# Optimization experiments

Measured on AMD Instinct MI355X. Metric: run time of the kernel, lower is better.

## Reference

```python
import jax, jax.numpy as jnp
import numpy as np
import math

B, S, E, H = 2, 2048, 1024, 16


def setup_inputs() -> dict:
    key = jax.random.key(0)
    ks = jax.random.split(key, 9)
    std = 0.02
    return {
        "x": jax.random.normal(ks[0], (B, S, E), dtype=jnp.float32),
        "Wq": jax.random.normal(ks[1], (E, E), dtype=jnp.float32) * std,
        "bq": jnp.zeros((E,), dtype=jnp.float32),
        "Wk": jax.random.normal(ks[2], (E, E), dtype=jnp.float32) * std,
        "bk": jnp.zeros((E,), dtype=jnp.float32),
        "Wv": jax.random.normal(ks[3], (E, E), dtype=jnp.float32) * std,
        "bv": jnp.zeros((E,), dtype=jnp.float32),
        "Wfc": jax.random.normal(ks[4], (E, E), dtype=jnp.float32) * std,
        "bfc": jnp.zeros((E,), dtype=jnp.float32),
        "n_head": H,
    }


def reference(x, Wq, bq, Wk, bk, Wv, bv, Wfc, bfc, n_head):
    Bn, Sn, En = x.shape
    Hd = En // n_head  # head_dim
    # torch Linear: y = x @ W.T + b
    def proj(W, b):
        return (x @ W.T + b).reshape(Bn, Sn, n_head, Hd).transpose(0, 2, 1, 3)  # [B,H,S,D]
    q = proj(Wq, bq)
    k = proj(Wk, bk)
    v = proj(Wv, bv)
    scores = jnp.einsum('bhqd,bhkd->bhqk', q, k) / math.sqrt(Hd)  # [B,H,S,S]
    # ALiBi: slopes_h = 2^{-(h+1)}; alibi[h,i,j] = -slope_h * (i - j)
    slopes = 2.0 ** (-jnp.arange(1, n_head + 1, dtype=jnp.float32))  # [H]
    pos = jnp.arange(Sn, dtype=jnp.float32)
    rel = pos[:, None] - pos[None, :]  # [S,S], memory_pos - context_pos
    alibi = -slopes[:, None, None] * rel  # [H,S,S]
    scores = scores + alibi[None]
    weights = jax.nn.softmax(scores, axis=-1)  # [B,H,S,S]
    out = jnp.einsum('bhqk,bhkd->bqhd', weights, v).reshape(Bn, Sn, En)
    out = out @ Wfc.T + bfc
    return (out, weights)
```

## Files before the change

### kernel.cpp

```cpp
#include <hip/hip_runtime.h>
#include <hip/hip_bf16.h>
#include <cstdint>
#include <cstddef>

#define BB 2
#define SS 2048
#define EE 1024
#define HH 16
#define MM (BB*SS)

typedef __bf16 bf16;
typedef __bf16 bf16x8 __attribute__((ext_vector_type(8)));
typedef float f32x4 __attribute__((ext_vector_type(4)));

#define GLD16(gsrc, ldst) \
  __builtin_amdgcn_global_load_lds((const __attribute__((address_space(1))) void*)(gsrc), \
                                   (__attribute__((address_space(3))) void*)(ldst), 16, 0, 0)

__global__ __launch_bounds__(256) void cvt_f32_bf16(const float* __restrict__ src,
                                                    bf16* __restrict__ dst, int n) {
    int i = (blockIdx.x * 256 + threadIdx.x) * 8;
    if (i >= n) return;
    float4 a = *(const float4*)(src + i);
    float4 b = *(const float4*)(src + i + 4);
    bf16 o[8] = {(bf16)a.x,(bf16)a.y,(bf16)a.z,(bf16)a.w,
                 (bf16)b.x,(bf16)b.y,(bf16)b.z,(bf16)b.w};
    *(uint4*)(dst + i) = *(uint4*)o;
}

__global__ __launch_bounds__(256) void cvt4(const float* __restrict__ a, const float* __restrict__ b,
                                            const float* __restrict__ c, const float* __restrict__ d,
                                            bf16* __restrict__ oa, bf16* __restrict__ ob,
                                            bf16* __restrict__ oc, bf16* __restrict__ od) {
    int sel = blockIdx.y;
    const float* s = sel == 0 ? a : sel == 1 ? b : sel == 2 ? c : d;
    bf16* o       = sel == 0 ? oa : sel == 1 ? ob : sel == 2 ? oc : od;
    int i = (blockIdx.x * 256 + threadIdx.x) * 8;
    float4 x = *(const float4*)(s + i);
    float4 y = *(const float4*)(s + i + 4);
    bf16 t[8] = {(bf16)x.x,(bf16)x.y,(bf16)x.z,(bf16)x.w,
                 (bf16)y.x,(bf16)y.y,(bf16)y.z,(bf16)y.w};
    *(uint4*)(o + i) = *(uint4*)t;
}

template<int MODE>
__global__ __launch_bounds__(256) void gemm128(const bf16* __restrict__ A,
                                               const bf16* __restrict__ W0,
                                               const bf16* __restrict__ W1,
                                               const bf16* __restrict__ W2,
                                               const float* __restrict__ b0,
                                               const float* __restrict__ b1,
                                               const float* __restrict__ b2,
                                               void* __restrict__ o0,
                                               void* __restrict__ o1,
                                               void* __restrict__ o2) {
    __shared__ bf16 Al[128*64];
    __shared__ bf16 Bl[128*64];
    const int t = threadIdx.x;
    const int wsel = blockIdx.x >> 3;
    const int n0 = (blockIdx.x & 7) * 128;
    const int m0 = blockIdx.y * 128;
    const bf16* W  = wsel == 0 ? W0 : wsel == 1 ? W1 : W2;
    const float* bias = wsel == 0 ? b0 : wsel == 1 ? b1 : b2;
    void* outp = wsel == 0 ? o0 : wsel == 1 ? o1 : o2;

    const int w = t >> 6, lane = t & 63, lg = lane >> 4, li = lane & 15;
    const int wr = w >> 1, wc = w & 1;
    f32x4 acc[4][4] = {};

    for (int k0 = 0; k0 < 1024; k0 += 64) {
        __syncthreads();
        #pragma unroll
        for (int i = 0; i < 4; ++i) {
            int f = i * 256 + t;
            int row = f >> 3, c = (f & 7) * 8;
            GLD16(A + (size_t)(m0 + row) * 1024 + k0 + c, Al + f * 8);
            GLD16(W + (size_t)(n0 + row) * 1024 + k0 + c, Bl + f * 8);
        }
        __syncthreads();
        #pragma unroll
        for (int ks = 0; ks < 2; ++ks) {
            bf16x8 af[4], bf_[4];
            #pragma unroll
            for (int m = 0; m < 4; ++m)
                af[m] = *(const bf16x8*)&Al[(wr*64 + m*16 + li)*64 + ks*32 + lg*8];
            #pragma unroll
            for (int n = 0; n < 4; ++n)
                bf_[n] = *(const bf16x8*)&Bl[(wc*64 + n*16 + li)*64 + ks*32 + lg*8];
            #pragma unroll
            for (int m = 0; m < 4; ++m)
                #pragma unroll
                for (int n = 0; n < 4; ++n)
                    acc[m][n] = __builtin_amdgcn_mfma_f32_16x16x32_bf16(af[m], bf_[n], acc[m][n], 0,0,0);
        }
    }
    #pragma unroll
    for (int m = 0; m < 4; ++m)
      #pragma unroll
      for (int n = 0; n < 4; ++n)
        #pragma unroll
        for (int r = 0; r < 4; ++r) {
            int row = m0 + wr*64 + m*16 + lg*4 + r;
            int col = n0 + wc*64 + n*16 + li;
            float v = acc[m][n][r] + bias[col];
            if (MODE == 0) {
                int b = row >> 11, s = row & (SS-1);
                int h = col >> 6, d = col & 63;
                ((bf16*)outp)[(((size_t)(b*HH + h)*SS + s) << 6) + d] = (bf16)v;
            } else {
                ((float*)outp)[(size_t)row*1024 + col] = v;
            }
        }
}

__global__ __launch_bounds__(256) void transpose_v(const bf16* __restrict__ V,
                                                   bf16* __restrict__ Vt) {
    __shared__ bf16 L[64][72];
    const int bh = blockIdx.y, s0 = blockIdx.x * 64, t = threadIdx.x;
    for (int id = t; id < 512; id += 256) {
        int row = id >> 3, c = id & 7;
        *(uint4*)&L[row][c*8] = *(const uint4*)&V[((size_t)bh*SS + s0 + row)*64 + c*8];
    }
    __syncthreads();
    for (int id = t; id < 512; id += 256) {
        int d = id >> 3, c = id & 7;
        bf16 tmp[8];
        #pragma unroll
        for (int jj = 0; jj < 8; ++jj) tmp[jj] = L[c*8 + jj][d];
        *(uint4*)&Vt[((size_t)bh*64 + d)*SS + s0 + c*8] = *(uint4*)tmp;
    }
}

__global__ __launch_bounds__(256) void attn1_kernel(const bf16* __restrict__ Q,
                                                    const bf16* __restrict__ Kk,
                                                    const bf16* __restrict__ Vt,
                                                    float* __restrict__ Lbuf,
                                                    bf16* __restrict__ aout) {
    __shared__ bf16 ring[4][64*64];
    __shared__ float Lred[2][64];

    const int lin = blockIdx.x + (int)(gridDim.x * blockIdx.y);
    const int nl  = (lin & 7) * 128 + (lin >> 3);
    const int qt = nl & 31, bh = nl >> 5;

    const int b = bh >> 4, h = bh & 15;
    const int q0 = qt * 64;
    const int t = threadIdx.x, w = t >> 6, lane = t & 63, lg = lane >> 4, li = lane & 15;
    const int jh = w & 1, qh = w >> 1;
    const float slope = exp2f(-(float)(h + 1));
    const size_t kvbase = (size_t)bh * SS * 64;
    const size_t vtbase = (size_t)bh * 64 * SS;
    const float L2E = 1.4426950408889634f;
    const float K1 = 0.125f * L2E;
    const float C  = slope * L2E;
    const float C64 = C * 64.f;

    bf16x8 aq[2][2];
    #pragma unroll
    for (int cbq = 0; cbq < 2; ++cbq) {
        const bf16* qptr = Q + kvbase + (size_t)(q0 + qh*32 + cbq*16 + li) * 64;
        aq[cbq][0] = *(const bf16x8*)(qptr + lg*8);
        aq[cbq][1] = *(const bf16x8*)(qptr + 32 + lg*8);
    }
    const int swz = (li & 7) << 4;

    #define STAGE_K(J0, DST) do {                                              \
        _Pragma("unroll")                                                      \
        for (int i_ = 0; i_ < 2; ++i_) {                                       \
            int f_ = i_*256 + t; int row_ = f_ >> 3, c_ = f_ & 7;              \
            GLD16(Kk + kvbase + (size_t)((J0) + row_)*64 + (c_ ^ (row_ & 7))*8,\
                  (DST) + f_*8);                                               \
        } } while (0)
    #define STAGE_V(J0, DST) do {                                              \
        _Pragma("unroll")                                                      \
        for (int i_ = 0; i_ < 2; ++i_) {                                       \
            int f_ = i_*256 + t; int row_ = f_ >> 3, c_ = f_ & 7;              \
            GLD16(Vt + vtbase + (size_t)row_*SS + (J0) + (c_ ^ (row_ & 7))*8,  \
                  (DST) + f_*8);                                               \
        } } while (0)

    float cj[2][4];
    #pragma unroll
    for (int jt = 0; jt < 2; ++jt)
        #pragma unroll
        for (int r = 0; r < 4; ++r)
            cj[jt][r] = C * (float)(jh*32 + jt*16 + lg*4 + r - (SS-1));
    float lp[2] = {0.f, 0.f};
    f32x4 acc[2][4] = {};

    STAGE_K(0, &ring[0][0]);
    STAGE_V(0, &ring[2][0]);
    __syncthreads();
    for (int kt = 0; kt < 32; ++kt) {
        const int cur = kt & 1;
        const int j0 = kt * 64;
        if (kt + 1 < 32) {
            STAGE_K(j0 + 64, &ring[cur ^ 1][0]);
            STAGE_V(j0 + 64, &ring[2 + (cur ^ 1)][0]);
        }
        const char* Ksb = (const char*)&ring[cur][0];
        const char* Vsb = (const char*)&ring[2 + cur][0];
        bf16x8 ak[2][2];
        #pragma unroll
        for (int jt = 0; jt < 2; ++jt) {
            int row = jh*32 + jt*16 + li;
            ak[jt][0] = *(const bf16x8*)(Ksb + row*128 + ((     lg*16) ^ swz));
            ak[jt][1] = *(const bf16x8*)(Ksb + row*128 + ((64 + lg*16) ^ swz));
        }
        f32x4 sc[2][2] = {};
        __builtin_amdgcn_s_setprio(1);
        #pragma unroll
        for (int jt = 0; jt < 2; ++jt)
            #pragma unroll
            for (int cbq = 0; cbq < 2; ++cbq) {
                sc[jt][cbq] = __builtin_amdgcn_mfma_f32_16x16x32_bf16(ak[jt][0], aq[cbq][0], sc[jt][cbq], 0,0,0);
                sc[jt][cbq] = __builtin_amdgcn_mfma_f32_16x16x32_bf16(ak[jt][1], aq[cbq][1], sc[jt][cbq], 0,0,0);
            }
        __builtin_amdgcn_s_setprio(0);
        f32x4 wv[2][2];
        #pragma unroll
        for (int jt = 0; jt < 2; ++jt) {
            #pragma unroll
            for (int cbq = 0; cbq < 2; ++cbq) {
                f32x4 v;
                #pragma unroll
                for (int r = 0; r < 4; ++r) {
                    v[r] = __builtin_amdgcn_exp2f(fmaf(sc[jt][cbq][r], K1, cj[jt][r]));
                    lp[cbq] += v[r];
                }
                wv[jt][cbq] = v;
            }
            #pragma unroll
            for (int r = 0; r < 4; ++r) cj[jt][r] += C64;
        }
        bf16x8 pa[2];
        #pragma unroll
        for (int cbq = 0; cbq < 2; ++cbq) {
            bf16x8 p;
            p[0] = (bf16)wv[0][cbq][0]; p[1] = (bf16)wv[0][cbq][1];
            p[2] = (bf16)wv[0][cbq][2]; p[3] = (bf16)wv[0][cbq][3];
            p[4] = (bf16)wv[1][cbq][0]; p[5] = (bf16)wv[1][cbq][1];
            p[6] = (bf16)wv[1][cbq][2]; p[7] = (bf16)wv[1][cbq][3];
            pa[cbq] = p;
        }
        bf16x8 vb[4];
        #pragma unroll
        for (int d0 = 0; d0 < 4; ++d0) {
            int row = d0*16 + li;
            uint2 u0 = *(const uint2*)(Vsb + row*128 + ((jh*64      + lg*8) ^ swz));
            uint2 u1 = *(const uint2*)(Vsb + row*128 + ((jh*64 + 32 + lg*8) ^ swz));
            uint4 uu = {u0.x, u0.y, u1.x, u1.y};
            vb[d0] = __builtin_bit_cast(bf16x8, uu);
        }
        __builtin_amdgcn_s_setprio(1);
        #pragma unroll
        for (int cbq = 0; cbq < 2; ++cbq)
            #pragma unroll
            for (int d0 = 0; d0 < 4; ++d0)
                acc[cbq][d0] = __builtin_amdgcn_mfma_f32_16x16x32_bf16(pa[cbq], vb[d0], acc[cbq][d0], 0,0,0);
        __builtin_amdgcn_s_setprio(0);
        __syncthreads();
    }
    #pragma unroll
    for (int cbq = 0; cbq < 2; ++cbq) {
        lp[cbq] += __shfl_xor(lp[cbq], 16);
        lp[cbq] += __shfl_xor(lp[cbq], 32);
    }
    if (lg == 0) {
        Lred[jh][qh*32 + li]      = lp[0];
        Lred[jh][qh*32 + 16 + li] = lp[1];
    }
    __syncthreads();
    if (t < 64) {
        float lv = Lred[0][t] + Lred[1][t];
        Lbuf[(size_t)bh*SS + q0 + t] = __builtin_amdgcn_logf(lv);
    }
    float rinv2[2][4];
    #pragma unroll
    for (int cbq = 0; cbq < 2; ++cbq)
        #pragma unroll
        for (int r = 0; r < 4; ++r) {
            int qi = qh*32 + cbq*16 + lg*4 + r;
            rinv2[cbq][r] = 1.f / (Lred[0][qi] + Lred[1][qi]);
        }
    __syncthreads();

    bf16* Obuf = &ring[0][0];
    #pragma unroll
    for (int cbq = 0; cbq < 2; ++cbq)
        #pragma unroll
        for (int d0 = 0; d0 < 4; ++d0)
            #pragma unroll
            for (int r = 0; r < 4; ++r)
                Obuf[jh*4096 + (qh*32 + cbq*16 + lg*4 + r)*64 + d0*16 + li] =
                    (bf16)(acc[cbq][d0][r] * rinv2[cbq][r]);
    __syncthreads();
    {
        int q = t >> 2, dc = (t & 3) << 4;
        const bf16* o0 = Obuf +        q*64 + dc;
        const bf16* o1 = Obuf + 4096 + q*64 + dc;
        bf16x8 a0 = *(const bf16x8*)(o0),     a1 = *(const bf16x8*)(o0 + 8);
        bf16x8 b0 = *(const bf16x8*)(o1),     b1 = *(const bf16x8*)(o1 + 8);
        bf16 ov[16];
        #pragma unroll
        for (int e = 0; e < 8; ++e) {
            ov[e]     = (bf16)((float)a0[e] + (float)b0[e]);
            ov[8 + e] = (bf16)((float)a1[e] + (float)b1[e]);
        }
        bf16* dst = aout + ((size_t)(b*SS + q0 + q))*EE + h*64 + dc;
        *(uint4*)(dst)     = *(uint4*)(ov);
        *(uint4*)(dst + 8) = *(uint4*)(ov + 8);
    }
    #undef STAGE_K
    #undef STAGE_V
}

__global__ __launch_bounds__(256) void weights_kernel(const bf16* __restrict__ Q,
                                                      const bf16* __restrict__ Kk,
                                                      const float* __restrict__ Lbuf,
                                                      float* __restrict__ wout) {
    const int lin = blockIdx.x + (int)(gridDim.x * blockIdx.y);
    const int nl  = (lin & 7) * 256 + (lin >> 3);
    const int bh = nl >> 6, rr = nl & 63;
    const int qt = rr >> 1, jc = rr & 1;

    const int h = bh & 15;
    const int q0 = qt * 64;
    const int jbase = jc * 1024;
    const int t = threadIdx.x, w = t >> 6, lane = t & 63, lg = lane >> 4, li = lane & 15;
    const int jh = w & 1, qh = w >> 1;
    const float slope = exp2f(-(float)(h + 1));
    const size_t kvbase = (size_t)bh * SS * 64;
    const float L2E = 1.4426950408889634f;
    const float K1 = 0.125f * L2E;
    const float C  = slope * L2E;
    const float C64 = C * 64.f;

    bf16x8 aq[2][2];
    float lgl[2];
    #pragma unroll
    for (int cbq = 0; cbq < 2; ++cbq) {
        const int qi = q0 + qh*32 + cbq*16 + li;
        const bf16* qptr = Q + kvbase + (size_t)qi * 64;
        aq[cbq][0] = *(const bf16x8*)(qptr + lg*8);
        aq[cbq][1] = *(const bf16x8*)(qptr + 32 + lg*8);
        lgl[cbq] = Lbuf[(size_t)bh*SS + qi];
    }
    float ecr[2][2][4];
    #pragma unroll
    for (int jt = 0; jt < 2; ++jt)
        #pragma unroll
        for (int cbq = 0; cbq < 2; ++cbq)
            #pragma unroll
            for (int r = 0; r < 4; ++r)
                ecr[jt][cbq][r] = C * (float)(jbase + jh*32 + jt*16 + lg*4 + r - (SS-1)) - lgl[cbq];

    float* wrow0 = wout + ((size_t)bh*SS + q0 + qh*32 +      li) * SS;
    float* wrow1 = wout + ((size_t)bh*SS + q0 + qh*32 + 16 + li) * SS;

    #pragma unroll 2
    for (int kt = 0; kt < 16; ++kt) {
        const int j0 = jbase + kt * 64;
        bf16x8 ak[2][2];
        #pragma unroll
        for (int jt = 0; jt < 2; ++jt) {
            const bf16* kr = Kk + kvbase + (size_t)(j0 + jh*32 + jt*16 + li) * 64;
            ak[jt][0] = *(const bf16x8*)(kr + lg*8);
            ak[jt][1] = *(const bf16x8*)(kr + 32 + lg*8);
        }
        f32x4 sc[2][2] = {};
        #pragma unroll
        for (int jt = 0; jt < 2; ++jt)
            #pragma unroll
            for (int cbq = 0; cbq < 2; ++cbq) {
                sc[jt][cbq] = __builtin_amdgcn_mfma_f32_16x16x32_bf16(ak[jt][0], aq[cbq][0], sc[jt][cbq], 0,0,0);
                sc[jt][cbq] = __builtin_amdgcn_mfma_f32_16x16x32_bf16(ak[jt][1], aq[cbq][1], sc[jt][cbq], 0,0,0);
            }
        #pragma unroll
        for (int jt = 0; jt < 2; ++jt)
            #pragma unroll
            for (int cbq = 0; cbq < 2; ++cbq) {
                f32x4 v;
                v[0] = __builtin_amdgcn_exp2f(fmaf(sc[jt][cbq][0], K1, ecr[jt][cbq][0]));
                v[1] = __builtin_amdgcn_exp2f(fmaf(sc[jt][cbq][1], K1, ecr[jt][cbq][1]));
                v[2] = __builtin_amdgcn_exp2f(fmaf(sc[jt][cbq][2], K1, ecr[jt][cbq][2]));
                v[3] = __builtin_amdgcn_exp2f(fmaf(sc[jt][cbq][3], K1, ecr[jt][cbq][3]));
                float* wr = (cbq == 0 ? wrow0 : wrow1);
                __builtin_nontemporal_store(v, (f32x4*)&wr[j0 + jh*32 + jt*16 + lg*4]);
                ecr[jt][cbq][0] += C64; ecr[jt][cbq][1] += C64;
                ecr[jt][cbq][2] += C64; ecr[jt][cbq][3] += C64;
            }
    }
}

extern "C" void kernel_launch(void* const* d_in, const int* in_sizes, int n_in,
                              void* d_out, int out_size, void* d_ws, size_t ws_size,
                              hipStream_t stream) {
    const float* x   = (const float*)d_in[0];
    const float* Wq  = (const float*)d_in[1];
    const float* bq  = (const float*)d_in[2];
    const float* Wk  = (const float*)d_in[3];
    const float* bk  = (const float*)d_in[4];
    const float* Wv  = (const float*)d_in[5];
    const float* bv  = (const float*)d_in[6];
    const float* Wfc = (const float*)d_in[7];
    const float* bfc = (const float*)d_in[8];

    char* ws = (char*)d_ws;
    const size_t MB = 1024u*1024u;
    bf16* xb   = (bf16*)(ws + 0);
    bf16* wqb  = (bf16*)(ws + 8*MB);
    bf16* wkb  = (bf16*)(ws + 10*MB);
    bf16* wvb  = (bf16*)(ws + 12*MB);
    bf16* wfb  = (bf16*)(ws + 14*MB);
    bf16* Qb   = (bf16*)(ws + 16*MB);
    bf16* Kb   = (bf16*)(ws + 24*MB);
    bf16* Vb   = (bf16*)(ws + 32*MB);
    bf16* Vtb  = (bf16*)(ws + 40*MB);
    bf16* Ab   = (bf16*)(ws + 48*MB);
    float* Lb  = (float*)(ws + 0);

    float* outp = (float*)d_out;
    float* wout = outp + (size_t)BB*SS*EE;

    cvt_f32_bf16<<<dim3(4194304/8/256), 256, 0, stream>>>(x, xb, 4194304);
    cvt4<<<dim3(512, 4), 256, 0, stream>>>(Wq, Wk, Wv, Wfc, wqb, wkb, wvb, wfb);

    gemm128<0><<<dim3(24, 32), 256, 0, stream>>>(xb, wqb, wkb, wvb, bq, bk, bv, Qb, Kb, Vb);

    transpose_v<<<dim3(SS/64, BB*HH), 256, 0, stream>>>(Vb, Vtb);

    attn1_kernel<<<dim3(32, 32), 256, 0, stream>>>(Qb, Kb, Vtb, Lb, Ab);

    weights_kernel<<<dim3(64, 32), 256, 0, stream>>>(Qb, Kb, Lb, wout);

    gemm128<1><<<dim3(8, 32), 256, 0, stream>>>(Ab, wfb, wfb, wfb, bfc, bfc, bfc, d_out, d_out, d_out);
}
```

Measured before the change: 341.4 us.

## Fuse PV into the weights-writing pass and split the key range across blocks

The attention stage is reorganised into four kernels. A light pass computes partial softmax denominators over two key halves, and a tiny kernel combines them into log-sums. The main kernel then writes the normalized attention weights and accumulates P·V in the same loop, each block handling half of the keys. A final kernel adds the two bf16 partial outputs. The goal is to overlap the PV MFMA work with the store-bound weights write and to double the number of blocks. In exchange it adds two small launches, extra partial-output traffic, and bf16 rounding of the partial sums.

New measurement: 319.8 us. 1.07x faster.

```diff
diff --git a/kernel.cpp b/kernel.cpp
--- a/kernel.cpp
+++ b/kernel.cpp
@@ -131,20 +131,127 @@
     }
 }
 
-__global__ __launch_bounds__(256) void attn1_kernel(const bf16* __restrict__ Q,
-                                                    const bf16* __restrict__ Kk,
-                                                    const bf16* __restrict__ Vt,
-                                                    float* __restrict__ Lbuf,
-                                                    bf16* __restrict__ aout) {
+__global__ __launch_bounds__(256) void lsum_kernel(const bf16* __restrict__ Q,
+                                                   const bf16* __restrict__ Kk,
+                                                   float* __restrict__ Lpart) {
+    __shared__ bf16 ring[2][64*64];
+    __shared__ float Lred[2][64];
+
+    const int lin = blockIdx.x + (int)(gridDim.x * blockIdx.y);
+    const int nl  = (lin & 7) * 256 + (lin >> 3);
+    const int bh = nl >> 6, rr = nl & 63;
+    const int qt = rr >> 1, jh2 = rr & 1;
+
+    const int h = bh & 15;
+    const int q0 = qt * 64;
+    const int jbase = jh2 * 1024;
+    const int t = threadIdx.x, w = t >> 6, lane = t & 63, lg = lane >> 4, li = lane & 15;
+    const int jh = w & 1, qh = w >> 1;
+    const float slope = exp2f(-(float)(h + 1));
+    const size_t kvbase = (size_t)bh * SS * 64;
+    const float L2E = 1.4426950408889634f;
+    const float K1 = 0.125f * L2E;
+    const float C  = slope * L2E;
+    const float C64 = C * 64.f;
+
+    bf16x8 aq[2][2];
+    #pragma unroll
+    for (int cbq = 0; cbq < 2; ++cbq) {
+        const bf16* qptr = Q + kvbase + (size_t)(q0 + qh*32 + cbq*16 + li) * 64;
+        aq[cbq][0] = *(const bf16x8*)(qptr + lg*8);
+        aq[cbq][1] = *(const bf16x8*)(qptr + 32 + lg*8);
+    }
+    const int swz = (li & 7) << 4;
+
+    #define STAGE_K(J0, DST) do {                                              \
+        _Pragma("unroll")                                                      \
+        for (int i_ = 0; i_ < 2; ++i_) {                                       \
+            int f_ = i_*256 + t; int row_ = f_ >> 3, c_ = f_ & 7;              \
+            GLD16(Kk + kvbase + (size_t)((J0) + row_)*64 + (c_ ^ (row_ & 7))*8,\
+                  (DST) + f_*8);                                               \
+        } } while (0)
+
+    float cj[2][4];
+    #pragma unroll
+    for (int jt = 0; jt < 2; ++jt)
+        #pragma unroll
+        for (int r = 0; r < 4; ++r)
+            cj[jt][r] = C * (float)(jbase + jh*32 + jt*16 + lg*4 + r - (SS-1));
+    float lp[2] = {0.f, 0.f};
+
+    STAGE_K(jbase, &ring[0][0]);
+    __syncthreads();
+    for (int kt = 0; kt < 16; ++kt) {
+        const int cur = kt & 1;
+        if (kt + 1 < 16) STAGE_K(jbase + (kt+1)*64, &ring[cur ^ 1][0]);
+        const char* Ksb = (const char*)&ring[cur][0];
+        bf16x8 ak[2][2];
+        #pragma unroll
+        for (int jt = 0; jt < 2; ++jt) {
+            int row = jh*32 + jt*16 + li;
+            ak[jt][0] = *(const bf16x8*)(Ksb + row*128 + ((     lg*16) ^ swz));
+            ak[jt][1] = *(const bf16x8*)(Ksb + row*128 + ((64 + lg*16) ^ swz));
+        }
+        f32x4 sc[2][2] = {};
+        __builtin_amdgcn_s_setprio(1);
+        #pragma unroll
+        for (int jt = 0; jt < 2; ++jt)
+            #pragma unroll
+            for (int cbq = 0; cbq < 2; ++cbq) {
+                sc[jt][cbq] = __builtin_amdgcn_mfma_f32_16x16x32_bf16(ak[jt][0], aq[cbq][0], sc[jt][cbq], 0,0,0);
+                sc[jt][cbq] = __builtin_amdgcn_mfma_f32_16x16x32_bf16(ak[jt][1], aq[cbq][1], sc[jt][cbq], 0,0,0);
+            }
+        __builtin_amdgcn_s_setprio(0);
+        #pragma unroll
+        for (int jt = 0; jt < 2; ++jt) {
+            #pragma unroll
+            for (int cbq = 0; cbq < 2; ++cbq)
+                #pragma unroll
+                for (int r = 0; r < 4; ++r)
+                    lp[cbq] += __builtin_amdgcn_exp2f(fmaf(sc[jt][cbq][r], K1, cj[jt][r]));
+            #pragma unroll
+            for (int r = 0; r < 4; ++r) cj[jt][r] += C64;
+        }
+        __syncthreads();
+    }
+    #pragma unroll
+    for (int cbq = 0; cbq < 2; ++cbq) {
+        lp[cbq] += __shfl_xor(lp[cbq], 16);
+        lp[cbq] += __shfl_xor(lp[cbq], 32);
+    }
+    if (lg == 0) {
+        Lred[jh][qh*32 + li]      = lp[0];
+        Lred[jh][qh*32 + 16 + li] = lp[1];
+    }
+    __syncthreads();
+    if (t < 64)
+        Lpart[((size_t)(jh2*32 + bh))*SS + q0 + t] = Lred[0][t] + Lred[1][t];
+    #undef STAGE_K
+}
+
+__global__ __launch_bounds__(1024) void lfix_kernel(const float* __restrict__ Lpart,
+                                                    float* __restrict__ Lbuf) {
+    int i = blockIdx.x * 1024 + threadIdx.x;
+    Lbuf[i] = __builtin_amdgcn_logf(Lpart[i] + Lpart[65536 + i]);
+}
+
+__global__ __launch_bounds__(256) void wpv_kernel(const bf16* __restrict__ Q,
+                                                  const bf16* __restrict__ Kk,
+                                                  const bf16* __restrict__ Vt,
+                                                  const float* __restrict__ Lbuf,
+                                                  float* __restrict__ wout,
+                                                  bf16* __restrict__ opart0,
+                                                  bf16* __restrict__ opart1) {
     __shared__ bf16 ring[4][64*64];
-    __shared__ float Lred[2][64];
 
     const int lin = blockIdx.x + (int)(gridDim.x * blockIdx.y);
-    const int nl  = (lin & 7) * 128 + (lin >> 3);
-    const int qt = nl & 31, bh = nl >> 5;
+    const int nl  = (lin & 7) * 256 + (lin >> 3);
+    const int bh = nl >> 6, rr = nl & 63;
+    const int qt = rr >> 1, jh2 = rr & 1;
 
     const int b = bh >> 4, h = bh & 15;
     const int q0 = qt * 64;
+    const int jbase = jh2 * 1024;
     const int t = threadIdx.x, w = t >> 6, lane = t & 63, lg = lane >> 4, li = lane & 15;
     const int jh = w & 1, qh = w >> 1;
     const float slope = exp2f(-(float)(h + 1));
@@ -154,13 +261,17 @@
     const float K1 = 0.125f * L2E;
     const float C  = slope * L2E;
     const float C64 = C * 64.f;
+    bf16* opart = jh2 == 0 ? opart0 : opart1;
 
     bf16x8 aq[2][2];
+    float lgl[2];
     #pragma unroll
     for (int cbq = 0; cbq < 2; ++cbq) {
-        const bf16* qptr = Q + kvbase + (size_t)(q0 + qh*32 + cbq*16 + li) * 64;
+        const int qi = q0 + qh*32 + cbq*16 + li;
+        const bf16* qptr = Q + kvbase + (size_t)qi * 64;
         aq[cbq][0] = *(const bf16x8*)(qptr + lg*8);
         aq[cbq][1] = *(const bf16x8*)(qptr + 32 + lg*8);
+        lgl[cbq] = Lbuf[(size_t)bh*SS + qi];
     }
     const int swz = (li & 7) << 4;
 
@@ -179,22 +290,26 @@
                   (DST) + f_*8);                                               \
         } } while (0)
 
-    float cj[2][4];
+    float ecr[2][2][4];
     #pragma unroll
     for (int jt = 0; jt < 2; ++jt)
         #pragma unroll
-        for (int r = 0; r < 4; ++r)
-            cj[jt][r] = C * (float)(jh*32 + jt*16 + lg*4 + r - (SS-1));
-    float lp[2] = {0.f, 0.f};
+        for (int cbq = 0; cbq < 2; ++cbq)
+            #pragma unroll
+            for (int r = 0; r < 4; ++r)
+                ecr[jt][cbq][r] = C * (float)(jbase + jh*32 + jt*16 + lg*4 + r - (SS-1)) - lgl[cbq];
+
     f32x4 acc[2][4] = {};
-
-    STAGE_K(0, &ring[0][0]);
-    STAGE_V(0, &ring[2][0]);
+    float* wrow0 = wout + ((size_t)bh*SS + q0 + qh*32 +      li) * SS;
+    float* wrow1 = wout + ((size_t)bh*SS + q0 + qh*32 + 16 + li) * SS;
+
+    STAGE_K(jbase, &ring[0][0]);
+    STAGE_V(jbase, &ring[2][0]);
     __syncthreads();
-    for (int kt = 0; kt < 32; ++kt) {
+    for (int kt = 0; kt < 16; ++kt) {
         const int cur = kt & 1;
-        const int j0 = kt * 64;
-        if (kt + 1 < 32) {
+        const int j0 = jbase + kt * 64;
+        if (kt + 1 < 16) {
             STAGE_K(j0 + 64, &ring[cur ^ 1][0]);
             STAGE_V(j0 + 64, &ring[2 + (cur ^ 1)][0]);
         }
@@ -219,20 +334,20 @@
         __builtin_amdgcn_s_setprio(0);
         f32x4 wv[2][2];
         #pragma unroll
-        for (int jt = 0; jt < 2; ++jt) {
+        for (int jt = 0; jt < 2; ++jt)
             #pragma unroll
             for (int cbq = 0; cbq < 2; ++cbq) {
                 f32x4 v;
-                #pragma unroll
-                for (int r = 0; r < 4; ++r) {
-                    v[r] = __builtin_amdgcn_exp2f(fmaf(sc[jt][cbq][r], K1, cj[jt][r]));
-                    lp[cbq] += v[r];
-                }
+                v[0] = __builtin_amdgcn_exp2f(fmaf(sc[jt][cbq][0], K1, ecr[jt][cbq][0]));
+                v[1] = __builtin_amdgcn_exp2f(fmaf(sc[jt][cbq][1], K1, ecr[jt][cbq][1]));
+                v[2] = __builtin_amdgcn_exp2f(fmaf(sc[jt][cbq][2], K1, ecr[jt][cbq][2]));
+                v[3] = __builtin_amdgcn_exp2f(fmaf(sc[jt][cbq][3], K1, ecr[jt][cbq][3]));
                 wv[jt][cbq] = v;
+                float* wr = (cbq == 0 ? wrow0 : wrow1);
+                __builtin_nontemporal_store(v, (f32x4*)&wr[j0 + jh*32 + jt*16 + lg*4]);
+                ecr[jt][cbq][0] += C64; ecr[jt][cbq][1] += C64;
+                ecr[jt][cbq][2] += C64; ecr[jt][cbq][3] += C64;
             }
-            #pragma unroll
-            for (int r = 0; r < 4; ++r) cj[jt][r] += C64;
-        }
         bf16x8 pa[2];
         #pragma unroll
         for (int cbq = 0; cbq < 2; ++cbq) {
@@ -261,29 +376,6 @@
         __builtin_amdgcn_s_setprio(0);
         __syncthreads();
     }
-    #pragma unroll
-    for (int cbq = 0; cbq < 2; ++cbq) {
-        lp[cbq] += __shfl_xor(lp[cbq], 16);
-        lp[cbq] += __shfl_xor(lp[cbq], 32);
-    }
-    if (lg == 0) {
-        Lred[jh][qh*32 + li]      = lp[0];
-        Lred[jh][qh*32 + 16 + li] = lp[1];
-    }
-    __syncthreads();
-    if (t < 64) {
-        float lv = Lred[0][t] + Lred[1][t];
-        Lbuf[(size_t)bh*SS + q0 + t] = __builtin_amdgcn_logf(lv);
-    }
-    float rinv2[2][4];
-    #pragma unroll
-    for (int cbq = 0; cbq < 2; ++cbq)
-        #pragma unroll
-        for (int r = 0; r < 4; ++r) {
-            int qi = qh*32 + cbq*16 + lg*4 + r;
-            rinv2[cbq][r] = 1.f / (Lred[0][qi] + Lred[1][qi]);
-        }
-    __syncthreads();
 
     bf16* Obuf = &ring[0][0];
     #pragma unroll
@@ -293,7 +385,7 @@
             #pragma unroll
             for (int r = 0; r < 4; ++r)
                 Obuf[jh*4096 + (qh*32 + cbq*16 + lg*4 + r)*64 + d0*16 + li] =
-                    (bf16)(acc[cbq][d0][r] * rinv2[cbq][r]);
+                    (bf16)acc[cbq][d0][r];
     __syncthreads();
     {
         int q = t >> 2, dc = (t & 3) << 4;
@@ -307,7 +399,7 @@
             ov[e]     = (bf16)((float)a0[e] + (float)b0[e]);
             ov[8 + e] = (bf16)((float)a1[e] + (float)b1[e]);
         }
-        bf16* dst = aout + ((size_t)(b*SS + q0 + q))*EE + h*64 + dc;
+        bf16* dst = opart + ((size_t)(b*SS + q0 + q))*EE + h*64 + dc;
         *(uint4*)(dst)     = *(uint4*)(ov);
         *(uint4*)(dst + 8) = *(uint4*)(ov + 8);
     }
@@ -315,82 +407,16 @@
     #undef STAGE_V
 }
 
-__global__ __launch_bounds__(256) void weights_kernel(const bf16* __restrict__ Q,
-                                                      const bf16* __restrict__ Kk,
-                                                      const float* __restrict__ Lbuf,
-                                                      float* __restrict__ wout) {
-    const int lin = blockIdx.x + (int)(gridDim.x * blockIdx.y);
-    const int nl  = (lin & 7) * 256 + (lin >> 3);
-    const int bh = nl >> 6, rr = nl & 63;
-    const int qt = rr >> 1, jc = rr & 1;
-
-    const int h = bh & 15;
-    const int q0 = qt * 64;
-    const int jbase = jc * 1024;
-    const int t = threadIdx.x, w = t >> 6, lane = t & 63, lg = lane >> 4, li = lane & 15;
-    const int jh = w & 1, qh = w >> 1;
-    const float slope = exp2f(-(float)(h + 1));
-    const size_t kvbase = (size_t)bh * SS * 64;
-    const float L2E = 1.4426950408889634f;
-    const float K1 = 0.125f * L2E;
-    const float C  = slope * L2E;
-    const float C64 = C * 64.f;
-
-    bf16x8 aq[2][2];
-    float lgl[2];
-    #pragma unroll
-    for (int cbq = 0; cbq < 2; ++cbq) {
-        const int qi = q0 + qh*32 + cbq*16 + li;
-        const bf16* qptr = Q + kvbase + (size_t)qi * 64;
-        aq[cbq][0] = *(const bf16x8*)(qptr + lg*8);
-        aq[cbq][1] = *(const bf16x8*)(qptr + 32 + lg*8);
-        lgl[cbq] = Lbuf[(size_t)bh*SS + qi];
-    }
-    float ecr[2][2][4];
-    #pragma unroll
-    for (int jt = 0; jt < 2; ++jt)
-        #pragma unroll
-        for (int cbq = 0; cbq < 2; ++cbq)
-            #pragma unroll
-            for (int r = 0; r < 4; ++r)
-                ecr[jt][cbq][r] = C * (float)(jbase + jh*32 + jt*16 + lg*4 + r - (SS-1)) - lgl[cbq];
-
-    float* wrow0 = wout + ((size_t)bh*SS + q0 + qh*32 +      li) * SS;
-    float* wrow1 = wout + ((size_t)bh*SS + q0 + qh*32 + 16 + li) * SS;
-
-    #pragma unroll 2
-    for (int kt = 0; kt < 16; ++kt) {
-        const int j0 = jbase + kt * 64;
-        bf16x8 ak[2][2];
-        #pragma unroll
-        for (int jt = 0; jt < 2; ++jt) {
-            const bf16* kr = Kk + kvbase + (size_t)(j0 + jh*32 + jt*16 + li) * 64;
-            ak[jt][0] = *(const bf16x8*)(kr + lg*8);
-            ak[jt][1] = *(const bf16x8*)(kr + 32 + lg*8);
-        }
-        f32x4 sc[2][2] = {};
-        #pragma unroll
-        for (int jt = 0; jt < 2; ++jt)
-            #pragma unroll
-            for (int cbq = 0; cbq < 2; ++cbq) {
-                sc[jt][cbq] = __builtin_amdgcn_mfma_f32_16x16x32_bf16(ak[jt][0], aq[cbq][0], sc[jt][cbq], 0,0,0);
-                sc[jt][cbq] = __builtin_amdgcn_mfma_f32_16x16x32_bf16(ak[jt][1], aq[cbq][1], sc[jt][cbq], 0,0,0);
-            }
-        #pragma unroll
-        for (int jt = 0; jt < 2; ++jt)
-            #pragma unroll
-            for (int cbq = 0; cbq < 2; ++cbq) {
-                f32x4 v;
-                v[0] = __builtin_amdgcn_exp2f(fmaf(sc[jt][cbq][0], K1, ecr[jt][cbq][0]));
-                v[1] = __builtin_amdgcn_exp2f(fmaf(sc[jt][cbq][1], K1, ecr[jt][cbq][1]));
-                v[2] = __builtin_amdgcn_exp2f(fmaf(sc[jt][cbq][2], K1, ecr[jt][cbq][2]));
-                v[3] = __builtin_amdgcn_exp2f(fmaf(sc[jt][cbq][3], K1, ecr[jt][cbq][3]));
-                float* wr = (cbq == 0 ? wrow0 : wrow1);
-                __builtin_nontemporal_store(v, (f32x4*)&wr[j0 + jh*32 + jt*16 + lg*4]);
-                ecr[jt][cbq][0] += C64; ecr[jt][cbq][1] += C64;
-                ecr[jt][cbq][2] += C64; ecr[jt][cbq][3] += C64;
-            }
-    }
+__global__ __launch_bounds__(256) void ored_kernel(const bf16* __restrict__ O0,
+                                                   const bf16* __restrict__ O1,
+                                                   bf16* __restrict__ Ab) {
+    int i = (blockIdx.x * 256 + threadIdx.x) * 8;
+    bf16x8 a = *(const bf16x8*)(O0 + i);
+    bf16x8 b = *(const bf16x8*)(O1 + i);
+    bf16 o[8];
+    #pragma unroll
+    for (int e = 0; e < 8; ++e) o[e] = (bf16)((float)a[e] + (float)b[e]);
+    *(uint4*)(Ab + i) = *(uint4*)o;
 }
 
 extern "C" void kernel_launch(void* const* d_in, const int* in_sizes, int n_in,
@@ -418,7 +444,10 @@
     bf16* Vb   = (bf16*)(ws + 32*MB);
     bf16* Vtb  = (bf16*)(ws + 40*MB);
     bf16* Ab   = (bf16*)(ws + 48*MB);
-    float* Lb  = (float*)(ws + 0);
+    bf16* Opart0 = (bf16*)(ws + 0);
+    bf16* Opart1 = (bf16*)(ws + 32*MB);
+    float* Lpart = (float*)(ws + 8*MB);
+    float* Lb    = (float*)(ws + 9*MB);
 
     float* outp = (float*)d_out;
     float* wout = outp + (size_t)BB*SS*EE;
@@ -430,9 +459,12 @@
 
     transpose_v<<<dim3(SS/64, BB*HH), 256, 0, stream>>>(Vb, Vtb);
 
-    attn1_kernel<<<dim3(32, 32), 256, 0, stream>>>(Qb, Kb, Vtb, Lb, Ab);
-
-    weights_kernel<<<dim3(64, 32), 256, 0, stream>>>(Qb, Kb, Lb, wout);
+    lsum_kernel<<<dim3(64, 32), 256, 0, stream>>>(Qb, Kb, Lpart);
+    lfix_kernel<<<dim3(64), 1024, 0, stream>>>(Lpart, Lb);
+
+    wpv_kernel<<<dim3(64, 32), 256, 0, stream>>>(Qb, Kb, Vtb, Lb, wout, Opart0, Opart1);
+
+    ored_kernel<<<dim3(2048), 256, 0, stream>>>(Opart0, Opart1, Ab);
 
     gemm128<1><<<dim3(8, 32), 256, 0, stream>>>(Ab, wfb, wfb, wfb, bfc, bfc, bfc, d_out, d_out, d_out);
 }
```
